# Kernel tuning notes

Measured on AMD Instinct MI355X. Metric: run time of the kernel, lower is better.

## Reference

```python
import math
import jax, jax.numpy as jnp
import numpy as np

N_HEADS = 8
EPS = 1e-6


def setup_inputs() -> dict:
    key = jax.random.key(0)
    k0, k1, k2, k3, k4 = jax.random.split(key, 5)
    B, T, E = 2, 1024, 512
    s = 1.0 / math.sqrt(E)
    x = jax.random.normal(k0, (B, T, E), dtype=jnp.float32)
    w_qkv = jax.random.normal(k1, (3 * E, E), dtype=jnp.float32) * s
    b_qkv = jax.random.normal(k2, (3 * E,), dtype=jnp.float32) * s
    w_out = jax.random.normal(k3, (E, E), dtype=jnp.float32) * s
    b_out = jax.random.normal(k4, (E,), dtype=jnp.float32) * s
    return {"x": x, "w_qkv": w_qkv, "b_qkv": b_qkv, "w_out": w_out, "b_out": b_out}


def reference(x, w_qkv, b_qkv, w_out, b_out):
    B, T, C = x.shape
    H = N_HEADS
    d = C // H

    qkv = x @ w_qkv.T + b_qkv                      # [B,T,3C]
    q, k, v = jnp.split(qkv, 3, axis=-1)

    def to_heads(t):
        return t.reshape(B, T, H, d).transpose(0, 2, 1, 3).astype(jnp.float32)  # [B,H,T,d]

    q, k, v = to_heads(q), to_heads(k), to_heads(v)

    pos = jnp.arange(T, dtype=jnp.float32)
    ang = (math.pi / 2) * pos / T
    cos_w = jnp.cos(ang)[None, None, :, None]      # [1,1,T,1]
    sin_w = jnp.sin(ang)[None, None, :, None]

    q_prime = jax.nn.relu(q)
    k_prime = jax.nn.relu(k)
    q_cos, q_sin = q_prime * cos_w, q_prime * sin_w
    k_cos, k_sin = k_prime * cos_w, k_prime * sin_w

    # causal linear attention via cumulative outer products (cosFormer)
    kv_cos_cs = jnp.cumsum(jnp.einsum('bhtd,bhte->bhtde', k_cos, v), axis=2)
    context = jnp.einsum('bhtd,bhtde->bhte', q_cos, kv_cos_cs)
    kv_sin_cs = jnp.cumsum(jnp.einsum('bhtd,bhte->bhtde', k_sin, v), axis=2)
    context = context + jnp.einsum('bhtd,bhtde->bhte', q_sin, kv_sin_cs)

    norm = (jnp.einsum('bhtd,bhtd->bht', q_cos, jnp.cumsum(k_cos, axis=2))
            + jnp.einsum('bhtd,bhtd->bht', q_sin, jnp.cumsum(k_sin, axis=2)))
    out = context / (norm[..., None] + EPS)        # [B,H,T,d]

    out = out.astype(x.dtype).transpose(0, 2, 1, 3).reshape(B, T, C)
    return out @ w_out.T + b_out
```

## Files before the change

### kernel.cpp

```cpp
#include <hip/hip_runtime.h>

typedef __bf16 bf16_t;
typedef __bf16 bf16x4 __attribute__((ext_vector_type(4)));
typedef __bf16 bf16x8 __attribute__((ext_vector_type(8)));
typedef float f32x4 __attribute__((ext_vector_type(4)));

#define T_SEQ 1024
#define EMB   512
#define NH    8
#define HD    64
#define BATCH 2
#define NBH   (BATCH*NH)
#define CHUNK 64
#define NCHUNK (T_SEQ/CHUNK)
#define NBLK  (NBH*NCHUNK)
#define LDA   72
#define LDK   68


__global__ __launch_bounds__(256) void cvt3_kernel(
    const float* __restrict__ x, const float* __restrict__ wq,
    const float* __restrict__ wo,
    bf16_t* __restrict__ xb, bf16_t* __restrict__ wqb, bf16_t* __restrict__ wob)
{
    int i = blockIdx.x * 256 + threadIdx.x;
    const float* s; bf16_t* d; int off;
    if (i < 262144)      { s = x;  d = xb;  off = i; }
    else if (i < 458752) { s = wq; d = wqb; off = i - 262144; }
    else                 { s = wo; d = wob; off = i - 458752; }
    float4 v = ((const float4*)s)[off];
    bf16x4 o;
    o[0] = (bf16_t)v.x; o[1] = (bf16_t)v.y;
    o[2] = (bf16_t)v.z; o[3] = (bf16_t)v.w;
    ((bf16x4*)d)[off] = o;
}

__global__ __launch_bounds__(256) void qkv_sum_kernel(
    const bf16_t* __restrict__ X, const bf16_t* __restrict__ W,
    const float* __restrict__ bias,
    bf16_t* __restrict__ qq, bf16_t* __restrict__ kk, bf16_t* __restrict__ vv,
    bf16_t* __restrict__ Ssc, bf16_t* __restrict__ Sss,
    float* __restrict__ zc, float* __restrict__ zs)
{
    __shared__ __align__(16) bf16_t sk[CHUNK * LDK];
    __shared__ __align__(16) bf16_t sv[CHUNK * LDK];
    __shared__ float cwt[CHUNK], swt[CHUNK];

    const int m0 = blockIdx.x * 64;
    const int h  = blockIdx.y;
    const int b  = m0 >> 10;
    const int ch = (m0 & 1023) >> 6;
    const int blk = (b * NH + h) * NCHUNK + ch;

    if (threadIdx.x < CHUNK) {
        int tg = ch * CHUNK + threadIdx.x;
        float ang = 1.5707963267948966f * (float)tg * (1.0f / (float)T_SEQ);
        cwt[threadIdx.x] = cosf(ang);
        swt[threadIdx.x] = sinf(ang);
    }

    const int w = threadIdx.x >> 6;
    const int lane = threadIdx.x & 63;
    if (w < 3) {
        const int rsel = lane & 15;
        const int koff = (lane >> 4) * 8;
        const int n0 = w * 512 + h * 64;
        f32x4 acc[4][4] = {};
        const bf16_t* Ap = X + (m0 + rsel) * EMB + koff;
        const bf16_t* Bp = W + (n0 + rsel) * EMB + koff;
#pragma unroll 4
        for (int k0 = 0; k0 < EMB; k0 += 32) {
            bf16x8 af[4], bfr[4];
            for (int i = 0; i < 4; ++i)
                af[i] = *(const bf16x8*)(Ap + i * 16 * EMB + k0);
            for (int j = 0; j < 4; ++j)
                bfr[j] = *(const bf16x8*)(Bp + j * 16 * EMB + k0);
            for (int i = 0; i < 4; ++i)
                for (int j = 0; j < 4; ++j)
                    acc[i][j] = __builtin_amdgcn_mfma_f32_16x16x32_bf16(
                        af[i], bfr[j], acc[i][j], 0, 0, 0);
        }
        for (int j = 0; j < 4; ++j) {
            const int feat = j * 16 + rsel;
            const float bn = bias[n0 + feat];
            for (int i = 0; i < 4; ++i) {
                const int tl0 = i * 16 + (lane >> 4) * 4;
                for (int r = 0; r < 4; ++r) {
                    const int tl = tl0 + r;
                    const int t = (m0 & 1023) + tl;
                    float val = acc[i][j][r] + bn;
                    int di = ((b * NH + h) * T_SEQ + t) * HD + feat;
                    if (w == 0) {
                        qq[di] = (bf16_t)fmaxf(val, 0.f);
                    } else if (w == 1) {
                        bf16_t kb = (bf16_t)fmaxf(val, 0.f);
                        kk[di] = kb;
                        sk[tl * LDK + feat] = kb;
                    } else {
                        bf16_t vb = (bf16_t)val;
                        vv[di] = vb;
                        sv[tl * LDK + feat] = vb;
                    }
                }
            }
        }
    }
    __syncthreads();

    const int i  = threadIdx.x & 63;
    const int jg = (threadIdx.x >> 6) * 16;
    float ac[16], as[16];
    for (int jj = 0; jj < 16; ++jj) { ac[jj] = 0.f; as[jj] = 0.f; }
    float zca = 0.f, zsa = 0.f;
    const bool zown = (jg == 0);
    for (int t = 0; t < CHUNK; ++t) {
        float kv = (float)sk[t * LDK + i];
        float kc_ = kv * cwt[t];
        float ks_ = kv * swt[t];
        if (zown) { zca += kc_; zsa += ks_; }
        for (int jj = 0; jj < 16; ++jj) {
            float vj = (float)sv[t * LDK + jg + jj];
            ac[jj] += kc_ * vj;
            as[jj] += ks_ * vj;
        }
    }
    bf16_t* oc = Ssc + blk * HD * HD;
    bf16_t* os = Sss + blk * HD * HD;
    for (int jj = 0; jj < 16; ++jj) {
        oc[(jg + jj) * HD + i] = (bf16_t)ac[jj];
        os[(jg + jj) * HD + i] = (bf16_t)as[jj];
    }
    if (zown) {
        zc[blk * HD + i] = zca;
        zs[blk * HD + i] = zsa;
    }
}

__global__ __launch_bounds__(256) void chunk_out_kernel(
    const bf16_t* __restrict__ qq, const bf16_t* __restrict__ kk,
    const bf16_t* __restrict__ vv,
    const bf16_t* __restrict__ SscT, const bf16_t* __restrict__ SssT,
    const float* __restrict__ zc, const float* __restrict__ zs,
    bf16_t* __restrict__ Y)
{
    const int blk = blockIdx.x;
    const int bh = blk >> 4, ch = blk & 15;
    __shared__ __align__(16) bf16_t sq [CHUNK * LDA];
    __shared__ __align__(16) bf16_t sk [CHUNK * LDA];
    __shared__ __align__(16) bf16_t svT[CHUNK * LDA];
    __shared__ __align__(16) bf16_t sct[CHUNK * LDA];
    __shared__ __align__(16) bf16_t sst[CHUNK * LDA];
    __shared__ __align__(16) bf16_t sp [CHUNK * LDA];
    __shared__ float cwt[CHUNK], swt[CHUNK], cosd[CHUNK];
    __shared__ float zcl[CHUNK], zsl[CHUNK], nrm[CHUNK];

    const int base = blk * CHUNK * HD;
    for (int i = threadIdx.x; i < CHUNK * HD / 8; i += 256) {
        int row = i >> 3, g = i & 7;
        ((uint4*)(sq + row * LDA))[g]  = ((const uint4*)(qq + base))[i];
        ((uint4*)(sk + row * LDA))[g]  = ((const uint4*)(kk + base))[i];
        bf16x8 v8 = *(const bf16x8*)(vv + base + i * 8);
        int t = i >> 3, bb = i & 7;
        int tg8 = t >> 3, tf = t & 7;
        for (int j = 0; j < 8; ++j) {
            int e = bb * 8 + j;
            int pg = (tg8 + bb) & 7;
            svT[e * LDA + pg * 8 + tf] = v8[j];
        }
    }
    {
        const int e0 = threadIdx.x * 16;
        float accC[16], accS[16];
        for (int j = 0; j < 16; ++j) { accC[j] = 0.f; accS[j] = 0.f; }
        const int sb = bh * NCHUNK * HD * HD + e0;
#pragma unroll 2
        for (int c = 0; c < ch; ++c) {
            const bf16x8* pc = (const bf16x8*)(SscT + sb + c * HD * HD);
            const bf16x8* ps = (const bf16x8*)(SssT + sb + c * HD * HD);
            bf16x8 c0 = pc[0], c1 = pc[1], s0 = ps[0], s1 = ps[1];
            for (int j = 0; j < 8; ++j) {
                accC[j] += (float)c0[j];  accC[8 + j] += (float)c1[j];
                accS[j] += (float)s0[j];  accS[8 + j] += (float)s1[j];
            }
        }
        const int row = threadIdx.x >> 2, col = (threadIdx.x & 3) * 16;
        bf16x8 oc0, oc1, os0, os1;
        for (int j = 0; j < 8; ++j) {
            oc0[j] = (bf16_t)accC[j];  oc1[j] = (bf16_t)accC[8 + j];
            os0[j] = (bf16_t)accS[j];  os1[j] = (bf16_t)accS[8 + j];
        }
        *(bf16x8*)(sct + row * LDA + col) = oc0;
        *(bf16x8*)(sct + row * LDA + col + 8) = oc1;
        *(bf16x8*)(sst + row * LDA + col) = os0;
        *(bf16x8*)(sst + row * LDA + col + 8) = os1;
    }
    if (threadIdx.x < HD) {
        int tl = threadIdx.x;
        float s = 0.f;
        for (int c = 0; c < ch; ++c) s += zc[(bh * NCHUNK + c) * HD + tl];
        zcl[tl] = s;
        int tg = ch * CHUNK + tl;
        float angg = 1.5707963267948966f * (float)tg * (1.0f / (float)T_SEQ);
        cwt[tl] = cosf(angg);
        swt[tl] = sinf(angg);
        cosd[tl] = cosf(1.5707963267948966f * (float)tl * (1.0f / (float)T_SEQ));
    } else if (threadIdx.x < 2 * HD) {
        int i = threadIdx.x - HD;
        float s = 0.f;
        for (int c = 0; c < ch; ++c) s += zs[(bh * NCHUNK + c) * HD + i];
        zsl[i] = s;
    }
    __syncthreads();

    const int w = threadIdx.x >> 6;
    const int lane = threadIdx.x & 63;
    const int rsel = lane & 15;
    const int koff = (lane >> 4) * 8;
    const int myrow = w * 16 + rsel;

    bf16x8 aq0 = *(const bf16x8*)(sq + myrow * LDA + koff);
    bf16x8 aq1 = *(const bf16x8*)(sq + myrow * LDA + koff + 32);
    for (int nt = 0; nt < 4; ++nt) {
        const int n0 = nt * 16;
        f32x4 pacc = {0.f, 0.f, 0.f, 0.f};
        bf16x8 b0 = *(const bf16x8*)(sk + (n0 + rsel) * LDA + koff);
        bf16x8 b1 = *(const bf16x8*)(sk + (n0 + rsel) * LDA + koff + 32);
        pacc = __builtin_amdgcn_mfma_f32_16x16x32_bf16(aq0, b0, pacc, 0, 0, 0);
        pacc = __builtin_amdgcn_mfma_f32_16x16x32_bf16(aq1, b1, pacc, 0, 0, 0);
        const int s = n0 + (lane & 15);
        const int tb = w * 16 + (lane >> 4) * 4;
        for (int r = 0; r < 4; ++r) {
            int t = tb + r;
            float p = (s <= t) ? pacc[r] * cosd[t - s] : 0.f;
            sp[t * LDA + s] = (bf16_t)p;
        }
    }

    if (lane < 16) {
        int row = w * 16 + lane;
        float nv = 0.f;
        const bf16x8* pr = (const bf16x8*)(sp + row * LDA);
        for (int g = 0; g < 8; ++g) {
            bf16x8 pv = pr[g];
            for (int j = 0; j < 8; ++j) nv += (float)pv[j];
        }
        float cwr = cwt[row], swr = swt[row];
        const bf16x8* qr = (const bf16x8*)(sq + row * LDA);
        for (int g = 0; g < 8; ++g) {
            bf16x8 qv = qr[g];
            for (int j = 0; j < 8; ++j)
                nv += (float)qv[j] * (cwr * zcl[g * 8 + j] + swr * zsl[g * 8 + j]);
        }
        nrm[row] = nv;
    }

    const float cwq = cwt[myrow], swq = swt[myrow];
    bf16x8 qc0, qc1, qs0, qs1;
    for (int j = 0; j < 8; ++j) {
        qc0[j] = (bf16_t)((float)aq0[j] * cwq);
        qc1[j] = (bf16_t)((float)aq1[j] * cwq);
        qs0[j] = (bf16_t)((float)aq0[j] * swq);
        qs1[j] = (bf16_t)((float)aq1[j] * swq);
    }
    bf16x8 ap0 = *(const bf16x8*)(sp + myrow * LDA + koff);
    bf16x8 ap1 = *(const bf16x8*)(sp + myrow * LDA + koff + 32);

    const int b = bh >> 3, h = bh & 7;
    const int g0 = koff >> 3;
    for (int nt = 0; nt < 4; ++nt) {
        const int n0 = nt * 16;
        const int ee = n0 + rsel;
        const int rot = (ee >> 3) & 7;
        const bf16_t* bvp0 = svT + ee * LDA + (((g0 + rot) & 7) << 3);
        const bf16_t* bvp1 = svT + ee * LDA + (((g0 + 4 + rot) & 7) << 3);
        const bf16_t* bcp = sct + ee * LDA + koff;
        const bf16_t* bsp = sst + ee * LDA + koff;
        f32x4 acc = {0.f, 0.f, 0.f, 0.f};
        acc = __builtin_amdgcn_mfma_f32_16x16x32_bf16(ap0, *(const bf16x8*)(bvp0), acc, 0, 0, 0);
        acc = __builtin_amdgcn_mfma_f32_16x16x32_bf16(ap1, *(const bf16x8*)(bvp1), acc, 0, 0, 0);
        acc = __builtin_amdgcn_mfma_f32_16x16x32_bf16(qc0, *(const bf16x8*)(bcp), acc, 0, 0, 0);
        acc = __builtin_amdgcn_mfma_f32_16x16x32_bf16(qc1, *(const bf16x8*)(bcp + 32), acc, 0, 0, 0);
        acc = __builtin_amdgcn_mfma_f32_16x16x32_bf16(qs0, *(const bf16x8*)(bsp), acc, 0, 0, 0);
        acc = __builtin_amdgcn_mfma_f32_16x16x32_bf16(qs1, *(const bf16x8*)(bsp + 32), acc, 0, 0, 0);
        const int col = n0 + (lane & 15);
        const int tb = w * 16 + (lane >> 4) * 4;
        for (int r = 0; r < 4; ++r) {
            int row = tb + r;
            float inv = 1.0f / (nrm[row] + 1e-6f);
            int tg = ch * CHUNK + row;
            Y[((b * T_SEQ + tg) * EMB) + h * HD + col] = (bf16_t)(acc[r] * inv);
        }
    }
}

__global__ __launch_bounds__(256) void out_gemm_kernel(
    const bf16_t* __restrict__ Yb, const bf16_t* __restrict__ W,
    const float* __restrict__ bias, float* __restrict__ out)
{
    const int w = threadIdx.x >> 6;
    const int lane = threadIdx.x & 63;
    const int rsel = lane & 15;
    const int koff = (lane >> 4) * 8;
    const int m0 = blockIdx.x * 64 + (w & 1) * 32;
    const int n0 = blockIdx.y * 64 + (w >> 1) * 32;
    f32x4 acc[2][2] = {};
    const bf16_t* Ap = Yb + (m0 + rsel) * EMB + koff;
    const bf16_t* Bp = W + (n0 + rsel) * EMB + koff;
#pragma unroll 8
    for (int k0 = 0; k0 < EMB; k0 += 32) {
        bf16x8 af[2], bfr[2];
        for (int i = 0; i < 2; ++i)
            af[i] = *(const bf16x8*)(Ap + i * 16 * EMB + k0);
        for (int j = 0; j < 2; ++j)
            bfr[j] = *(const bf16x8*)(Bp + j * 16 * EMB + k0);
        for (int i = 0; i < 2; ++i)
            for (int j = 0; j < 2; ++j)
                acc[i][j] = __builtin_amdgcn_mfma_f32_16x16x32_bf16(
                    af[i], bfr[j], acc[i][j], 0, 0, 0);
    }
    for (int j = 0; j < 2; ++j) {
        const int n = n0 + j * 16 + rsel;
        const float bn = bias[n];
        for (int i = 0; i < 2; ++i) {
            const int mb = m0 + i * 16 + (lane >> 4) * 4;
            for (int r = 0; r < 4; ++r)
                out[(mb + r) * EMB + n] = acc[i][j][r] + bn;
        }
    }
}

extern "C" void kernel_launch(void* const* d_in, const int* in_sizes, int n_in,
                              void* d_out, int out_size, void* d_ws, size_t ws_size,
                              hipStream_t stream) {
    const float* x     = (const float*)d_in[0];
    const float* w_qkv = (const float*)d_in[1];
    const float* b_qkv = (const float*)d_in[2];
    const float* w_out = (const float*)d_in[3];
    const float* b_out = (const float*)d_in[4];
    float* out = (float*)d_out;

    char* w = (char*)d_ws;
    const size_t N_X   = (size_t)BATCH * T_SEQ * EMB;
    const size_t N_WQ  = (size_t)3 * EMB * EMB;
    const size_t N_WO  = (size_t)EMB * EMB;
    bf16_t* xb   = (bf16_t*)w;                 w += N_X  * sizeof(bf16_t);
    bf16_t* wqb  = (bf16_t*)w;                 w += N_WQ * sizeof(bf16_t);
    bf16_t* wob  = (bf16_t*)w;                 w += N_WO * sizeof(bf16_t);
    const size_t SZ_BHTD = (size_t)NBH * T_SEQ * HD * sizeof(bf16_t);
    bf16_t* qq = (bf16_t*)w;                   w += SZ_BHTD;
    bf16_t* kk = (bf16_t*)w;                   w += SZ_BHTD;
    bf16_t* vv = (bf16_t*)w;                   w += SZ_BHTD;
    bf16_t* Y  = (bf16_t*)w;                   w += SZ_BHTD;
    bf16_t* SscT = (bf16_t*)w;                 w += (size_t)NBLK * HD * HD * sizeof(bf16_t);
    bf16_t* SssT = (bf16_t*)w;                 w += (size_t)NBLK * HD * HD * sizeof(bf16_t);
    float* zc = (float*)w;                     w += (size_t)NBLK * HD * sizeof(float);
    float* zs = (float*)w;

    cvt3_kernel<<<2048, 256, 0, stream>>>(x, w_qkv, w_out, xb, wqb, wob);
    qkv_sum_kernel<<<dim3(32, 8), 256, 0, stream>>>(
        xb, wqb, b_qkv, qq, kk, vv, SscT, SssT, zc, zs);
    chunk_out_kernel<<<NBLK, 256, 0, stream>>>(qq, kk, vv, SscT, SssT, zc, zs, Y);
    out_gemm_kernel<<<dim3(2048 / 64, 512 / 64), 256, 0, stream>>>(
        Y, wob, b_out, out);
}
```

Before: 118.8 us.

## Fuse all four stages into one cooperative kernel with grid syncs

Merges the conversion, QKV GEMM plus chunk-sum, chunk output, and output GEMM kernels into a single cooperative launch of 256 blocks. Grid-wide barriers separate the stages, and one shared-memory union is reused across phases. The goal is to remove per-kernel launch gaps and tail effects between four small kernels. The cost is grid.sync overhead and the conversion phase running on only 256 blocks instead of 2048.

```diff
diff --git a/kernel.cpp b/kernel.cpp
--- a/kernel.cpp
+++ b/kernel.cpp
@@ -1,4 +1,7 @@
 #include <hip/hip_runtime.h>
+#include <hip/hip_cooperative_groups.h>
+
+namespace cg = cooperative_groups;
 
 typedef __bf16 bf16_t;
 typedef __bf16 bf16x4 __attribute__((ext_vector_type(4)));
@@ -18,313 +21,329 @@
 #define LDK   68
 
 
-__global__ __launch_bounds__(256) void cvt3_kernel(
-    const float* __restrict__ x, const float* __restrict__ wq,
-    const float* __restrict__ wo,
-    bf16_t* __restrict__ xb, bf16_t* __restrict__ wqb, bf16_t* __restrict__ wob)
-{
-    int i = blockIdx.x * 256 + threadIdx.x;
-    const float* s; bf16_t* d; int off;
-    if (i < 262144)      { s = x;  d = xb;  off = i; }
-    else if (i < 458752) { s = wq; d = wqb; off = i - 262144; }
-    else                 { s = wo; d = wob; off = i - 458752; }
-    float4 v = ((const float4*)s)[off];
-    bf16x4 o;
-    o[0] = (bf16_t)v.x; o[1] = (bf16_t)v.y;
-    o[2] = (bf16_t)v.z; o[3] = (bf16_t)v.w;
-    ((bf16x4*)d)[off] = o;
-}
-
-__global__ __launch_bounds__(256) void qkv_sum_kernel(
-    const bf16_t* __restrict__ X, const bf16_t* __restrict__ W,
-    const float* __restrict__ bias,
+struct P1s {
+    bf16_t sk[CHUNK * LDK];
+    bf16_t sv[CHUNK * LDK];
+    float  cwt[CHUNK], swt[CHUNK];
+};
+struct P2s {
+    bf16_t sq [CHUNK * LDA];
+    bf16_t sk [CHUNK * LDA];
+    bf16_t svT[CHUNK * LDA];
+    bf16_t sct[CHUNK * LDA];
+    bf16_t sst[CHUNK * LDA];
+    bf16_t sp [CHUNK * LDA];
+    float  cwt[CHUNK], swt[CHUNK], cosd[CHUNK];
+    float  zcl[CHUNK], zsl[CHUNK], nrm[CHUNK];
+};
+union SMemU { P1s p1; P2s p2; };
+
+__global__ __launch_bounds__(256) void fused_kernel(
+    const float* __restrict__ x,  const float* __restrict__ wq,
+    const float* __restrict__ wo, const float* __restrict__ b_qkv,
+    const float* __restrict__ b_out,
+    bf16_t* __restrict__ xb, bf16_t* __restrict__ wqb, bf16_t* __restrict__ wob,
     bf16_t* __restrict__ qq, bf16_t* __restrict__ kk, bf16_t* __restrict__ vv,
     bf16_t* __restrict__ Ssc, bf16_t* __restrict__ Sss,
-    float* __restrict__ zc, float* __restrict__ zs)
+    float* __restrict__ zc, float* __restrict__ zs,
+    bf16_t* __restrict__ Y, float* __restrict__ out)
 {
-    __shared__ __align__(16) bf16_t sk[CHUNK * LDK];
-    __shared__ __align__(16) bf16_t sv[CHUNK * LDK];
-    __shared__ float cwt[CHUNK], swt[CHUNK];
-
-    const int m0 = blockIdx.x * 64;
-    const int h  = blockIdx.y;
-    const int b  = m0 >> 10;
-    const int ch = (m0 & 1023) >> 6;
-    const int blk = (b * NH + h) * NCHUNK + ch;
-
-    if (threadIdx.x < CHUNK) {
-        int tg = ch * CHUNK + threadIdx.x;
-        float ang = 1.5707963267948966f * (float)tg * (1.0f / (float)T_SEQ);
-        cwt[threadIdx.x] = cosf(ang);
-        swt[threadIdx.x] = sinf(ang);
+    __shared__ __align__(16) SMemU sm;
+    cg::grid_group grid = cg::this_grid();
+    const int tid = threadIdx.x;
+    const int blk = blockIdx.x;
+
+    for (int i = blk * 256 + tid; i < 524288; i += NBLK * 256) {
+        const float* s; bf16_t* d; int off;
+        if (i < 262144)      { s = x;  d = xb;  off = i; }
+        else if (i < 458752) { s = wq; d = wqb; off = i - 262144; }
+        else                 { s = wo; d = wob; off = i - 458752; }
+        float4 v = ((const float4*)s)[off];
+        bf16x4 o;
+        o[0] = (bf16_t)v.x; o[1] = (bf16_t)v.y;
+        o[2] = (bf16_t)v.z; o[3] = (bf16_t)v.w;
+        ((bf16x4*)d)[off] = o;
     }
-
-    const int w = threadIdx.x >> 6;
-    const int lane = threadIdx.x & 63;
-    if (w < 3) {
+    grid.sync();
+
+    {
+        bf16_t* sk  = sm.p1.sk;
+        bf16_t* sv  = sm.p1.sv;
+        float*  cwt = sm.p1.cwt;
+        float*  swt = sm.p1.swt;
+
+        const int m0 = (blk & 31) * 64;
+        const int h  = blk >> 5;
+        const int b  = m0 >> 10;
+        const int ch = (m0 & 1023) >> 6;
+        const int sblk = (b * NH + h) * NCHUNK + ch;
+
+        if (tid < CHUNK) {
+            int tg = ch * CHUNK + tid;
+            float ang = 1.5707963267948966f * (float)tg * (1.0f / (float)T_SEQ);
+            cwt[tid] = cosf(ang);
+            swt[tid] = sinf(ang);
+        }
+
+        const int w = tid >> 6;
+        const int lane = tid & 63;
+        if (w < 3) {
+            const int rsel = lane & 15;
+            const int koff = (lane >> 4) * 8;
+            const int n0 = w * 512 + h * 64;
+            f32x4 acc[4][4] = {};
+            const bf16_t* Ap = xb + (m0 + rsel) * EMB + koff;
+            const bf16_t* Bp = wqb + (n0 + rsel) * EMB + koff;
+#pragma unroll 4
+            for (int k0 = 0; k0 < EMB; k0 += 32) {
+                bf16x8 af[4], bfr[4];
+                for (int i = 0; i < 4; ++i)
+                    af[i] = *(const bf16x8*)(Ap + i * 16 * EMB + k0);
+                for (int j = 0; j < 4; ++j)
+                    bfr[j] = *(const bf16x8*)(Bp + j * 16 * EMB + k0);
+                for (int i = 0; i < 4; ++i)
+                    for (int j = 0; j < 4; ++j)
+                        acc[i][j] = __builtin_amdgcn_mfma_f32_16x16x32_bf16(
+                            af[i], bfr[j], acc[i][j], 0, 0, 0);
+            }
+            for (int j = 0; j < 4; ++j) {
+                const int feat = j * 16 + rsel;
+                const float bn = b_qkv[n0 + feat];
+                for (int i = 0; i < 4; ++i) {
+                    const int tl0 = i * 16 + (lane >> 4) * 4;
+                    for (int r = 0; r < 4; ++r) {
+                        const int tl = tl0 + r;
+                        const int t = (m0 & 1023) + tl;
+                        float val = acc[i][j][r] + bn;
+                        int di = ((b * NH + h) * T_SEQ + t) * HD + feat;
+                        if (w == 0) {
+                            qq[di] = (bf16_t)fmaxf(val, 0.f);
+                        } else if (w == 1) {
+                            bf16_t kb = (bf16_t)fmaxf(val, 0.f);
+                            kk[di] = kb;
+                            sk[tl * LDK + feat] = kb;
+                        } else {
+                            bf16_t vb = (bf16_t)val;
+                            vv[di] = vb;
+                            sv[tl * LDK + feat] = vb;
+                        }
+                    }
+                }
+            }
+        }
+        __syncthreads();
+
+        const int il = tid & 63;
+        const int jg = (tid >> 6) * 16;
+        float ac[16], as[16];
+        for (int jj = 0; jj < 16; ++jj) { ac[jj] = 0.f; as[jj] = 0.f; }
+        float zca = 0.f, zsa = 0.f;
+        const bool zown = (jg == 0);
+        for (int t = 0; t < CHUNK; ++t) {
+            float kv = (float)sk[t * LDK + il];
+            float kc_ = kv * cwt[t];
+            float ks_ = kv * swt[t];
+            if (zown) { zca += kc_; zsa += ks_; }
+            for (int jj = 0; jj < 16; ++jj) {
+                float vj = (float)sv[t * LDK + jg + jj];
+                ac[jj] += kc_ * vj;
+                as[jj] += ks_ * vj;
+            }
+        }
+        bf16_t* oc = Ssc + sblk * HD * HD;
+        bf16_t* os = Sss + sblk * HD * HD;
+        for (int jj = 0; jj < 16; ++jj) {
+            oc[(jg + jj) * HD + il] = (bf16_t)ac[jj];
+            os[(jg + jj) * HD + il] = (bf16_t)as[jj];
+        }
+        if (zown) {
+            zc[sblk * HD + il] = zca;
+            zs[sblk * HD + il] = zsa;
+        }
+    }
+    grid.sync();
+
+    {
+        const int bh = blk >> 4, ch = blk & 15;
+        bf16_t* sq  = sm.p2.sq;
+        bf16_t* skl = sm.p2.sk;
+        bf16_t* svT = sm.p2.svT;
+        bf16_t* sct = sm.p2.sct;
+        bf16_t* sst = sm.p2.sst;
+        bf16_t* sp  = sm.p2.sp;
+        float* cwt = sm.p2.cwt; float* swt = sm.p2.swt; float* cosd = sm.p2.cosd;
+        float* zcl = sm.p2.zcl; float* zsl = sm.p2.zsl; float* nrm = sm.p2.nrm;
+
+        const int base = blk * CHUNK * HD;
+        for (int i = tid; i < CHUNK * HD / 8; i += 256) {
+            int row = i >> 3, g = i & 7;
+            ((uint4*)(sq + row * LDA))[g]  = ((const uint4*)(qq + base))[i];
+            ((uint4*)(skl + row * LDA))[g] = ((const uint4*)(kk + base))[i];
+            bf16x8 v8 = *(const bf16x8*)(vv + base + i * 8);
+            int t = i >> 3, bb = i & 7;
+            int tg8 = t >> 3, tf = t & 7;
+            for (int j = 0; j < 8; ++j) {
+                int e = bb * 8 + j;
+                int pg = (tg8 + bb) & 7;
+                svT[e * LDA + pg * 8 + tf] = v8[j];
+            }
+        }
+        {
+            const int e0 = tid * 16;
+            float accC[16], accS[16];
+            for (int j = 0; j < 16; ++j) { accC[j] = 0.f; accS[j] = 0.f; }
+            const int sb = bh * NCHUNK * HD * HD + e0;
+#pragma unroll 2
+            for (int c = 0; c < ch; ++c) {
+                const bf16x8* pc = (const bf16x8*)(Ssc + sb + c * HD * HD);
+                const bf16x8* ps = (const bf16x8*)(Sss + sb + c * HD * HD);
+                bf16x8 c0 = pc[0], c1 = pc[1], s0 = ps[0], s1 = ps[1];
+                for (int j = 0; j < 8; ++j) {
+                    accC[j] += (float)c0[j];  accC[8 + j] += (float)c1[j];
+                    accS[j] += (float)s0[j];  accS[8 + j] += (float)s1[j];
+                }
+            }
+            const int row = tid >> 2, col = (tid & 3) * 16;
+            bf16x8 oc0, oc1, os0, os1;
+            for (int j = 0; j < 8; ++j) {
+                oc0[j] = (bf16_t)accC[j];  oc1[j] = (bf16_t)accC[8 + j];
+                os0[j] = (bf16_t)accS[j];  os1[j] = (bf16_t)accS[8 + j];
+            }
+            *(bf16x8*)(sct + row * LDA + col) = oc0;
+            *(bf16x8*)(sct + row * LDA + col + 8) = oc1;
+            *(bf16x8*)(sst + row * LDA + col) = os0;
+            *(bf16x8*)(sst + row * LDA + col + 8) = os1;
+        }
+        if (tid < HD) {
+            int tl = tid;
+            float s = 0.f;
+            for (int c = 0; c < ch; ++c) s += zc[(bh * NCHUNK + c) * HD + tl];
+            zcl[tl] = s;
+            int tg = ch * CHUNK + tl;
+            float angg = 1.5707963267948966f * (float)tg * (1.0f / (float)T_SEQ);
+            cwt[tl] = cosf(angg);
+            swt[tl] = sinf(angg);
+            cosd[tl] = cosf(1.5707963267948966f * (float)tl * (1.0f / (float)T_SEQ));
+        } else if (tid < 2 * HD) {
+            int i = tid - HD;
+            float s = 0.f;
+            for (int c = 0; c < ch; ++c) s += zs[(bh * NCHUNK + c) * HD + i];
+            zsl[i] = s;
+        }
+        __syncthreads();
+
+        const int w = tid >> 6;
+        const int lane = tid & 63;
         const int rsel = lane & 15;
         const int koff = (lane >> 4) * 8;
-        const int n0 = w * 512 + h * 64;
-        f32x4 acc[4][4] = {};
-        const bf16_t* Ap = X + (m0 + rsel) * EMB + koff;
-        const bf16_t* Bp = W + (n0 + rsel) * EMB + koff;
-#pragma unroll 4
+        const int myrow = w * 16 + rsel;
+
+        bf16x8 aq0 = *(const bf16x8*)(sq + myrow * LDA + koff);
+        bf16x8 aq1 = *(const bf16x8*)(sq + myrow * LDA + koff + 32);
+        for (int nt = 0; nt < 4; ++nt) {
+            const int n0 = nt * 16;
+            f32x4 pacc = {0.f, 0.f, 0.f, 0.f};
+            bf16x8 b0 = *(const bf16x8*)(skl + (n0 + rsel) * LDA + koff);
+            bf16x8 b1 = *(const bf16x8*)(skl + (n0 + rsel) * LDA + koff + 32);
+            pacc = __builtin_amdgcn_mfma_f32_16x16x32_bf16(aq0, b0, pacc, 0, 0, 0);
+            pacc = __builtin_amdgcn_mfma_f32_16x16x32_bf16(aq1, b1, pacc, 0, 0, 0);
+            const int s = n0 + (lane & 15);
+            const int tb = w * 16 + (lane >> 4) * 4;
+            for (int r = 0; r < 4; ++r) {
+                int t = tb + r;
+                float p = (s <= t) ? pacc[r] * cosd[t - s] : 0.f;
+                sp[t * LDA + s] = (bf16_t)p;
+            }
+        }
+
+        if (lane < 16) {
+            int row = w * 16 + lane;
+            float nv = 0.f;
+            const bf16x8* pr = (const bf16x8*)(sp + row * LDA);
+            for (int g = 0; g < 8; ++g) {
+                bf16x8 pv = pr[g];
+                for (int j = 0; j < 8; ++j) nv += (float)pv[j];
+            }
+            float cwr = cwt[row], swr = swt[row];
+            const bf16x8* qr = (const bf16x8*)(sq + row * LDA);
+            for (int g = 0; g < 8; ++g) {
+                bf16x8 qv = qr[g];
+                for (int j = 0; j < 8; ++j)
+                    nv += (float)qv[j] * (cwr * zcl[g * 8 + j] + swr * zsl[g * 8 + j]);
+            }
+            nrm[row] = nv;
+        }
+
+        const float cwq = cwt[myrow], swq = swt[myrow];
+        bf16x8 qc0, qc1, qs0, qs1;
+        for (int j = 0; j < 8; ++j) {
+            qc0[j] = (bf16_t)((float)aq0[j] * cwq);
+            qc1[j] = (bf16_t)((float)aq1[j] * cwq);
+            qs0[j] = (bf16_t)((float)aq0[j] * swq);
+            qs1[j] = (bf16_t)((float)aq1[j] * swq);
+        }
+        bf16x8 ap0 = *(const bf16x8*)(sp + myrow * LDA + koff);
+        bf16x8 ap1 = *(const bf16x8*)(sp + myrow * LDA + koff + 32);
+
+        const int b = bh >> 3, h = bh & 7;
+        const int g0 = koff >> 3;
+        for (int nt = 0; nt < 4; ++nt) {
+            const int n0 = nt * 16;
+            const int ee = n0 + rsel;
+            const int rot = (ee >> 3) & 7;
+            const bf16_t* bvp0 = svT + ee * LDA + (((g0 + rot) & 7) << 3);
+            const bf16_t* bvp1 = svT + ee * LDA + (((g0 + 4 + rot) & 7) << 3);
+            const bf16_t* bcp = sct + ee * LDA + koff;
+            const bf16_t* bsp = sst + ee * LDA + koff;
+            f32x4 acc = {0.f, 0.f, 0.f, 0.f};
+            acc = __builtin_amdgcn_mfma_f32_16x16x32_bf16(ap0, *(const bf16x8*)(bvp0), acc, 0, 0, 0);
+            acc = __builtin_amdgcn_mfma_f32_16x16x32_bf16(ap1, *(const bf16x8*)(bvp1), acc, 0, 0, 0);
+            acc = __builtin_amdgcn_mfma_f32_16x16x32_bf16(qc0, *(const bf16x8*)(bcp), acc, 0, 0, 0);
+            acc = __builtin_amdgcn_mfma_f32_16x16x32_bf16(qc1, *(const bf16x8*)(bcp + 32), acc, 0, 0, 0);
+            acc = __builtin_amdgcn_mfma_f32_16x16x32_bf16(qs0, *(const bf16x8*)(bsp), acc, 0, 0, 0);
+            acc = __builtin_amdgcn_mfma_f32_16x16x32_bf16(qs1, *(const bf16x8*)(bsp + 32), acc, 0, 0, 0);
+            const int col = n0 + (lane & 15);
+            const int tb = w * 16 + (lane >> 4) * 4;
+            for (int r = 0; r < 4; ++r) {
+                int row = tb + r;
+                float inv = 1.0f / (nrm[row] + 1e-6f);
+                int tg = ch * CHUNK + row;
+                Y[((b * T_SEQ + tg) * EMB) + h * HD + col] = (bf16_t)(acc[r] * inv);
+            }
+        }
+    }
+    grid.sync();
+
+    {
+        const int w = tid >> 6;
+        const int lane = tid & 63;
+        const int rsel = lane & 15;
+        const int koff = (lane >> 4) * 8;
+        const int m0 = (blk & 31) * 64 + (w & 1) * 32;
+        const int n0 = (blk >> 5) * 64 + (w >> 1) * 32;
+        f32x4 acc[2][2] = {};
+        const bf16_t* Ap = Y + (m0 + rsel) * EMB + koff;
+        const bf16_t* Bp = wob + (n0 + rsel) * EMB + koff;
+#pragma unroll 8
         for (int k0 = 0; k0 < EMB; k0 += 32) {
-            bf16x8 af[4], bfr[4];
-            for (int i = 0; i < 4; ++i)
+            bf16x8 af[2], bfr[2];
+            for (int i = 0; i < 2; ++i)
                 af[i] = *(const bf16x8*)(Ap + i * 16 * EMB + k0);
-            for (int j = 0; j < 4; ++j)
+            for (int j = 0; j < 2; ++j)
                 bfr[j] = *(const bf16x8*)(Bp + j * 16 * EMB + k0);
-            for (int i = 0; i < 4; ++i)
-                for (int j = 0; j < 4; ++j)
+            for (int i = 0; i < 2; ++i)
+                for (int j = 0; j < 2; ++j)
                     acc[i][j] = __builtin_amdgcn_mfma_f32_16x16x32_bf16(
                         af[i], bfr[j], acc[i][j], 0, 0, 0);
         }
-        for (int j = 0; j < 4; ++j) {
-            const int feat = j * 16 + rsel;
-            const float bn = bias[n0 + feat];
-            for (int i = 0; i < 4; ++i) {
-                const int tl0 = i * 16 + (lane >> 4) * 4;
-                for (int r = 0; r < 4; ++r) {
-                    const int tl = tl0 + r;
-                    const int t = (m0 & 1023) + tl;
-                    float val = acc[i][j][r] + bn;
-                    int di = ((b * NH + h) * T_SEQ + t) * HD + feat;
-                    if (w == 0) {
-                        qq[di] = (bf16_t)fmaxf(val, 0.f);
-                    } else if (w == 1) {
-                        bf16_t kb = (bf16_t)fmaxf(val, 0.f);
-                        kk[di] = kb;
-                        sk[tl * LDK + feat] = kb;
-                    } else {
-                        bf16_t vb = (bf16_t)val;
-                        vv[di] = vb;
-                        sv[tl * LDK + feat] = vb;
-                    }
-                }
-            }
-        }
-    }
-    __syncthreads();
-
-    const int i  = threadIdx.x & 63;
-    const int jg = (threadIdx.x >> 6) * 16;
-    float ac[16], as[16];
-    for (int jj = 0; jj < 16; ++jj) { ac[jj] = 0.f; as[jj] = 0.f; }
-    float zca = 0.f, zsa = 0.f;
-    const bool zown = (jg == 0);
-    for (int t = 0; t < CHUNK; ++t) {
-        float kv = (float)sk[t * LDK + i];
-        float kc_ = kv * cwt[t];
-        float ks_ = kv * swt[t];
-        if (zown) { zca += kc_; zsa += ks_; }
-        for (int jj = 0; jj < 16; ++jj) {
-            float vj = (float)sv[t * LDK + jg + jj];
-            ac[jj] += kc_ * vj;
-            as[jj] += ks_ * vj;
-        }
-    }
-    bf16_t* oc = Ssc + blk * HD * HD;
-    bf16_t* os = Sss + blk * HD * HD;
-    for (int jj = 0; jj < 16; ++jj) {
-        oc[(jg + jj) * HD + i] = (bf16_t)ac[jj];
-        os[(jg + jj) * HD + i] = (bf16_t)as[jj];
-    }
-    if (zown) {
-        zc[blk * HD + i] = zca;
-        zs[blk * HD + i] = zsa;
-    }
-}
-
-__global__ __launch_bounds__(256) void chunk_out_kernel(
-    const bf16_t* __restrict__ qq, const bf16_t* __restrict__ kk,
-    const bf16_t* __restrict__ vv,
-    const bf16_t* __restrict__ SscT, const bf16_t* __restrict__ SssT,
-    const float* __restrict__ zc, const float* __restrict__ zs,
-    bf16_t* __restrict__ Y)
-{
-    const int blk = blockIdx.x;
-    const int bh = blk >> 4, ch = blk & 15;
-    __shared__ __align__(16) bf16_t sq [CHUNK * LDA];
-    __shared__ __align__(16) bf16_t sk [CHUNK * LDA];
-    __shared__ __align__(16) bf16_t svT[CHUNK * LDA];
-    __shared__ __align__(16) bf16_t sct[CHUNK * LDA];
-    __shared__ __align__(16) bf16_t sst[CHUNK * LDA];
-    __shared__ __align__(16) bf16_t sp [CHUNK * LDA];
-    __shared__ float cwt[CHUNK], swt[CHUNK], cosd[CHUNK];
-    __shared__ float zcl[CHUNK], zsl[CHUNK], nrm[CHUNK];
-
-    const int base = blk * CHUNK * HD;
-    for (int i = threadIdx.x; i < CHUNK * HD / 8; i += 256) {
-        int row = i >> 3, g = i & 7;
-        ((uint4*)(sq + row * LDA))[g]  = ((const uint4*)(qq + base))[i];
-        ((uint4*)(sk + row * LDA))[g]  = ((const uint4*)(kk + base))[i];
-        bf16x8 v8 = *(const bf16x8*)(vv + base + i * 8);
-        int t = i >> 3, bb = i & 7;
-        int tg8 = t >> 3, tf = t & 7;
-        for (int j = 0; j < 8; ++j) {
-            int e = bb * 8 + j;
-            int pg = (tg8 + bb) & 7;
-            svT[e * LDA + pg * 8 + tf] = v8[j];
-        }
-    }
-    {
-        const int e0 = threadIdx.x * 16;
-        float accC[16], accS[16];
-        for (int j = 0; j < 16; ++j) { accC[j] = 0.f; accS[j] = 0.f; }
-        const int sb = bh * NCHUNK * HD * HD + e0;
-#pragma unroll 2
-        for (int c = 0; c < ch; ++c) {
-            const bf16x8* pc = (const bf16x8*)(SscT + sb + c * HD * HD);
-            const bf16x8* ps = (const bf16x8*)(SssT + sb + c * HD * HD);
-            bf16x8 c0 = pc[0], c1 = pc[1], s0 = ps[0], s1 = ps[1];
-            for (int j = 0; j < 8; ++j) {
-                accC[j] += (float)c0[j];  accC[8 + j] += (float)c1[j];
-                accS[j] += (float)s0[j];  accS[8 + j] += (float)s1[j];
-            }
-        }
-        const int row = threadIdx.x >> 2, col = (threadIdx.x & 3) * 16;
-        bf16x8 oc0, oc1, os0, os1;
-        for (int j = 0; j < 8; ++j) {
-            oc0[j] = (bf16_t)accC[j];  oc1[j] = (bf16_t)accC[8 + j];
-            os0[j] = (bf16_t)accS[j];  os1[j] = (bf16_t)accS[8 + j];
-        }
-        *(bf16x8*)(sct + row * LDA + col) = oc0;
-        *(bf16x8*)(sct + row * LDA + col + 8) = oc1;
-        *(bf16x8*)(sst + row * LDA + col) = os0;
-        *(bf16x8*)(sst + row * LDA + col + 8) = os1;
-    }
-    if (threadIdx.x < HD) {
-        int tl = threadIdx.x;
-        float s = 0.f;
-        for (int c = 0; c < ch; ++c) s += zc[(bh * NCHUNK + c) * HD + tl];
-        zcl[tl] = s;
-        int tg = ch * CHUNK + tl;
-        float angg = 1.5707963267948966f * (float)tg * (1.0f / (float)T_SEQ);
-        cwt[tl] = cosf(angg);
-        swt[tl] = sinf(angg);
-        cosd[tl] = cosf(1.5707963267948966f * (float)tl * (1.0f / (float)T_SEQ));
-    } else if (threadIdx.x < 2 * HD) {
-        int i = threadIdx.x - HD;
-        float s = 0.f;
-        for (int c = 0; c < ch; ++c) s += zs[(bh * NCHUNK + c) * HD + i];
-        zsl[i] = s;
-    }
-    __syncthreads();
-
-    const int w = threadIdx.x >> 6;
-    const int lane = threadIdx.x & 63;
-    const int rsel = lane & 15;
-    const int koff = (lane >> 4) * 8;
-    const int myrow = w * 16 + rsel;
-
-    bf16x8 aq0 = *(const bf16x8*)(sq + myrow * LDA + koff);
-    bf16x8 aq1 = *(const bf16x8*)(sq + myrow * LDA + koff + 32);
-    for (int nt = 0; nt < 4; ++nt) {
-        const int n0 = nt * 16;
-        f32x4 pacc = {0.f, 0.f, 0.f, 0.f};
-        bf16x8 b0 = *(const bf16x8*)(sk + (n0 + rsel) * LDA + koff);
-        bf16x8 b1 = *(const bf16x8*)(sk + (n0 + rsel) * LDA + koff + 32);
-        pacc = __builtin_amdgcn_mfma_f32_16x16x32_bf16(aq0, b0, pacc, 0, 0, 0);
-        pacc = __builtin_amdgcn_mfma_f32_16x16x32_bf16(aq1, b1, pacc, 0, 0, 0);
-        const int s = n0 + (lane & 15);
-        const int tb = w * 16 + (lane >> 4) * 4;
-        for (int r = 0; r < 4; ++r) {
-            int t = tb + r;
-            float p = (s <= t) ? pacc[r] * cosd[t - s] : 0.f;
-            sp[t * LDA + s] = (bf16_t)p;
-        }
-    }
-
-    if (lane < 16) {
-        int row = w * 16 + lane;
-        float nv = 0.f;
-        const bf16x8* pr = (const bf16x8*)(sp + row * LDA);
-        for (int g = 0; g < 8; ++g) {
-            bf16x8 pv = pr[g];
-            for (int j = 0; j < 8; ++j) nv += (float)pv[j];
-        }
-        float cwr = cwt[row], swr = swt[row];
-        const bf16x8* qr = (const bf16x8*)(sq + row * LDA);
-        for (int g = 0; g < 8; ++g) {
-            bf16x8 qv = qr[g];
-            for (int j = 0; j < 8; ++j)
-                nv += (float)qv[j] * (cwr * zcl[g * 8 + j] + swr * zsl[g * 8 + j]);
-        }
-        nrm[row] = nv;
-    }
-
-    const float cwq = cwt[myrow], swq = swt[myrow];
-    bf16x8 qc0, qc1, qs0, qs1;
-    for (int j = 0; j < 8; ++j) {
-        qc0[j] = (bf16_t)((float)aq0[j] * cwq);
-        qc1[j] = (bf16_t)((float)aq1[j] * cwq);
-        qs0[j] = (bf16_t)((float)aq0[j] * swq);
-        qs1[j] = (bf16_t)((float)aq1[j] * swq);
-    }
-    bf16x8 ap0 = *(const bf16x8*)(sp + myrow * LDA + koff);
-    bf16x8 ap1 = *(const bf16x8*)(sp + myrow * LDA + koff + 32);
-
-    const int b = bh >> 3, h = bh & 7;
-    const int g0 = koff >> 3;
-    for (int nt = 0; nt < 4; ++nt) {
-        const int n0 = nt * 16;
-        const int ee = n0 + rsel;
-        const int rot = (ee >> 3) & 7;
-        const bf16_t* bvp0 = svT + ee * LDA + (((g0 + rot) & 7) << 3);
-        const bf16_t* bvp1 = svT + ee * LDA + (((g0 + 4 + rot) & 7) << 3);
-        const bf16_t* bcp = sct + ee * LDA + koff;
-        const bf16_t* bsp = sst + ee * LDA + koff;
-        f32x4 acc = {0.f, 0.f, 0.f, 0.f};
-        acc = __builtin_amdgcn_mfma_f32_16x16x32_bf16(ap0, *(const bf16x8*)(bvp0), acc, 0, 0, 0);
-        acc = __builtin_amdgcn_mfma_f32_16x16x32_bf16(ap1, *(const bf16x8*)(bvp1), acc, 0, 0, 0);
-        acc = __builtin_amdgcn_mfma_f32_16x16x32_bf16(qc0, *(const bf16x8*)(bcp), acc, 0, 0, 0);
-        acc = __builtin_amdgcn_mfma_f32_16x16x32_bf16(qc1, *(const bf16x8*)(bcp + 32), acc, 0, 0, 0);
-        acc = __builtin_amdgcn_mfma_f32_16x16x32_bf16(qs0, *(const bf16x8*)(bsp), acc, 0, 0, 0);
-        acc = __builtin_amdgcn_mfma_f32_16x16x32_bf16(qs1, *(const bf16x8*)(bsp + 32), acc, 0, 0, 0);
-        const int col = n0 + (lane & 15);
-        const int tb = w * 16 + (lane >> 4) * 4;
-        for (int r = 0; r < 4; ++r) {
-            int row = tb + r;
-            float inv = 1.0f / (nrm[row] + 1e-6f);
-            int tg = ch * CHUNK + row;
-            Y[((b * T_SEQ + tg) * EMB) + h * HD + col] = (bf16_t)(acc[r] * inv);
-        }
-    }
-}
-
-__global__ __launch_bounds__(256) void out_gemm_kernel(
-    const bf16_t* __restrict__ Yb, const bf16_t* __restrict__ W,
-    const float* __restrict__ bias, float* __restrict__ out)
-{
-    const int w = threadIdx.x >> 6;
-    const int lane = threadIdx.x & 63;
-    const int rsel = lane & 15;
-    const int koff = (lane >> 4) * 8;
-    const int m0 = blockIdx.x * 64 + (w & 1) * 32;
-    const int n0 = blockIdx.y * 64 + (w >> 1) * 32;
-    f32x4 acc[2][2] = {};
-    const bf16_t* Ap = Yb + (m0 + rsel) * EMB + koff;
-    const bf16_t* Bp = W + (n0 + rsel) * EMB + koff;
-#pragma unroll 8
-    for (int k0 = 0; k0 < EMB; k0 += 32) {
-        bf16x8 af[2], bfr[2];
-        for (int i = 0; i < 2; ++i)
-            af[i] = *(const bf16x8*)(Ap + i * 16 * EMB + k0);
-        for (int j = 0; j < 2; ++j)
-            bfr[j] = *(const bf16x8*)(Bp + j * 16 * EMB + k0);
-        for (int i = 0; i < 2; ++i)
-            for (int j = 0; j < 2; ++j)
-                acc[i][j] = __builtin_amdgcn_mfma_f32_16x16x32_bf16(
-                    af[i], bfr[j], acc[i][j], 0, 0, 0);
-    }
-    for (int j = 0; j < 2; ++j) {
-        const int n = n0 + j * 16 + rsel;
-        const float bn = bias[n];
-        for (int i = 0; i < 2; ++i) {
-            const int mb = m0 + i * 16 + (lane >> 4) * 4;
-            for (int r = 0; r < 4; ++r)
-                out[(mb + r) * EMB + n] = acc[i][j][r] + bn;
+        for (int j = 0; j < 2; ++j) {
+            const int n = n0 + j * 16 + rsel;
+            const float bn = b_out[n];
+            for (int i = 0; i < 2; ++i) {
+                const int mb = m0 + i * 16 + (lane >> 4) * 4;
+                for (int r = 0; r < 4; ++r)
+                    out[(mb + r) * EMB + n] = acc[i][j][r] + bn;
+            }
         }
     }
 }
@@ -356,10 +375,13 @@
     float* zc = (float*)w;                     w += (size_t)NBLK * HD * sizeof(float);
     float* zs = (float*)w;
 
-    cvt3_kernel<<<2048, 256, 0, stream>>>(x, w_qkv, w_out, xb, wqb, wob);
-    qkv_sum_kernel<<<dim3(32, 8), 256, 0, stream>>>(
-        xb, wqb, b_qkv, qq, kk, vv, SscT, SssT, zc, zs);
-    chunk_out_kernel<<<NBLK, 256, 0, stream>>>(qq, kk, vv, SscT, SssT, zc, zs, Y);
-    out_gemm_kernel<<<dim3(2048 / 64, 512 / 64), 256, 0, stream>>>(
-        Y, wob, b_out, out);
+    void* args[] = {
+        (void*)&x, (void*)&w_qkv, (void*)&w_out, (void*)&b_qkv, (void*)&b_out,
+        (void*)&xb, (void*)&wqb, (void*)&wob,
+        (void*)&qq, (void*)&kk, (void*)&vv,
+        (void*)&SscT, (void*)&SssT, (void*)&zc, (void*)&zs,
+        (void*)&Y, (void*)&out
+    };
+    hipLaunchCooperativeKernel((const void*)fused_kernel, dim3(NBLK), dim3(256),
+                               args, 0, stream);
 }
```

New measurement: 218.6 us. 83.9% more time.

## Fuse fp32-to-bf16 conversion into GEMM loads and retile output GEMM

Applied to the files above, without the earlier changes.

Removes the separate conversion kernel and has the QKV and output GEMMs read fp32 inputs and weights directly, converting to bf16 in registers before the MFMA. This drops one kernel launch and a full round trip of bf16 copies through memory. In exchange each GEMM reads twice as many bytes per operand, and the weights are converted redundantly by every block. The output GEMM also drops to one 16-row tile per wave and launches twice as many blocks, giving more parallelism but less register reuse.

```diff
diff --git a/kernel.cpp b/kernel.cpp
--- a/kernel.cpp
+++ b/kernel.cpp
@@ -18,25 +18,17 @@
 #define LDK   68
 
 
-__global__ __launch_bounds__(256) void cvt3_kernel(
-    const float* __restrict__ x, const float* __restrict__ wq,
-    const float* __restrict__ wo,
-    bf16_t* __restrict__ xb, bf16_t* __restrict__ wqb, bf16_t* __restrict__ wob)
-{
-    int i = blockIdx.x * 256 + threadIdx.x;
-    const float* s; bf16_t* d; int off;
-    if (i < 262144)      { s = x;  d = xb;  off = i; }
-    else if (i < 458752) { s = wq; d = wqb; off = i - 262144; }
-    else                 { s = wo; d = wob; off = i - 458752; }
-    float4 v = ((const float4*)s)[off];
-    bf16x4 o;
-    o[0] = (bf16_t)v.x; o[1] = (bf16_t)v.y;
-    o[2] = (bf16_t)v.z; o[3] = (bf16_t)v.w;
-    ((bf16x4*)d)[off] = o;
+__device__ __forceinline__ bf16x8 cvt8(const float* __restrict__ p) {
+    float4 a = *(const float4*)p;
+    float4 b = *(const float4*)(p + 4);
+    bf16x8 r;
+    r[0] = (bf16_t)a.x; r[1] = (bf16_t)a.y; r[2] = (bf16_t)a.z; r[3] = (bf16_t)a.w;
+    r[4] = (bf16_t)b.x; r[5] = (bf16_t)b.y; r[6] = (bf16_t)b.z; r[7] = (bf16_t)b.w;
+    return r;
 }
 
 __global__ __launch_bounds__(256) void qkv_sum_kernel(
-    const bf16_t* __restrict__ X, const bf16_t* __restrict__ W,
+    const float* __restrict__ X, const float* __restrict__ W,
     const float* __restrict__ bias,
     bf16_t* __restrict__ qq, bf16_t* __restrict__ kk, bf16_t* __restrict__ vv,
     bf16_t* __restrict__ Ssc, bf16_t* __restrict__ Sss,
@@ -66,15 +58,15 @@
         const int koff = (lane >> 4) * 8;
         const int n0 = w * 512 + h * 64;
         f32x4 acc[4][4] = {};
-        const bf16_t* Ap = X + (m0 + rsel) * EMB + koff;
-        const bf16_t* Bp = W + (n0 + rsel) * EMB + koff;
-#pragma unroll 4
+        const float* Ap = X + (m0 + rsel) * EMB + koff;
+        const float* Bp = W + (n0 + rsel) * EMB + koff;
+#pragma unroll 2
         for (int k0 = 0; k0 < EMB; k0 += 32) {
             bf16x8 af[4], bfr[4];
             for (int i = 0; i < 4; ++i)
-                af[i] = *(const bf16x8*)(Ap + i * 16 * EMB + k0);
+                af[i] = cvt8(Ap + i * 16 * EMB + k0);
             for (int j = 0; j < 4; ++j)
-                bfr[j] = *(const bf16x8*)(Bp + j * 16 * EMB + k0);
+                bfr[j] = cvt8(Bp + j * 16 * EMB + k0);
             for (int i = 0; i < 4; ++i)
                 for (int j = 0; j < 4; ++j)
                     acc[i][j] = __builtin_amdgcn_mfma_f32_16x16x32_bf16(
@@ -294,38 +286,34 @@
 }
 
 __global__ __launch_bounds__(256) void out_gemm_kernel(
-    const bf16_t* __restrict__ Yb, const bf16_t* __restrict__ W,
+    const bf16_t* __restrict__ Yb, const float* __restrict__ W,
     const float* __restrict__ bias, float* __restrict__ out)
 {
     const int w = threadIdx.x >> 6;
     const int lane = threadIdx.x & 63;
     const int rsel = lane & 15;
     const int koff = (lane >> 4) * 8;
-    const int m0 = blockIdx.x * 64 + (w & 1) * 32;
+    const int m0 = blockIdx.x * 32 + (w & 1) * 16;
     const int n0 = blockIdx.y * 64 + (w >> 1) * 32;
-    f32x4 acc[2][2] = {};
+    f32x4 acc[2] = {};
     const bf16_t* Ap = Yb + (m0 + rsel) * EMB + koff;
-    const bf16_t* Bp = W + (n0 + rsel) * EMB + koff;
-#pragma unroll 8
+    const float* Bp = W + (n0 + rsel) * EMB + koff;
+#pragma unroll 4
     for (int k0 = 0; k0 < EMB; k0 += 32) {
-        bf16x8 af[2], bfr[2];
-        for (int i = 0; i < 2; ++i)
-            af[i] = *(const bf16x8*)(Ap + i * 16 * EMB + k0);
+        bf16x8 af = *(const bf16x8*)(Ap + k0);
+        bf16x8 bfr[2];
         for (int j = 0; j < 2; ++j)
-            bfr[j] = *(const bf16x8*)(Bp + j * 16 * EMB + k0);
-        for (int i = 0; i < 2; ++i)
-            for (int j = 0; j < 2; ++j)
-                acc[i][j] = __builtin_amdgcn_mfma_f32_16x16x32_bf16(
-                    af[i], bfr[j], acc[i][j], 0, 0, 0);
+            bfr[j] = cvt8(Bp + j * 16 * EMB + k0);
+        for (int j = 0; j < 2; ++j)
+            acc[j] = __builtin_amdgcn_mfma_f32_16x16x32_bf16(
+                af, bfr[j], acc[j], 0, 0, 0);
     }
     for (int j = 0; j < 2; ++j) {
         const int n = n0 + j * 16 + rsel;
         const float bn = bias[n];
-        for (int i = 0; i < 2; ++i) {
-            const int mb = m0 + i * 16 + (lane >> 4) * 4;
-            for (int r = 0; r < 4; ++r)
-                out[(mb + r) * EMB + n] = acc[i][j][r] + bn;
-        }
+        const int mb = m0 + (lane >> 4) * 4;
+        for (int r = 0; r < 4; ++r)
+            out[(mb + r) * EMB + n] = acc[j][r] + bn;
     }
 }
 
@@ -340,12 +328,6 @@
     float* out = (float*)d_out;
 
     char* w = (char*)d_ws;
-    const size_t N_X   = (size_t)BATCH * T_SEQ * EMB;
-    const size_t N_WQ  = (size_t)3 * EMB * EMB;
-    const size_t N_WO  = (size_t)EMB * EMB;
-    bf16_t* xb   = (bf16_t*)w;                 w += N_X  * sizeof(bf16_t);
-    bf16_t* wqb  = (bf16_t*)w;                 w += N_WQ * sizeof(bf16_t);
-    bf16_t* wob  = (bf16_t*)w;                 w += N_WO * sizeof(bf16_t);
     const size_t SZ_BHTD = (size_t)NBH * T_SEQ * HD * sizeof(bf16_t);
     bf16_t* qq = (bf16_t*)w;                   w += SZ_BHTD;
     bf16_t* kk = (bf16_t*)w;                   w += SZ_BHTD;
@@ -356,10 +338,9 @@
     float* zc = (float*)w;                     w += (size_t)NBLK * HD * sizeof(float);
     float* zs = (float*)w;
 
-    cvt3_kernel<<<2048, 256, 0, stream>>>(x, w_qkv, w_out, xb, wqb, wob);
     qkv_sum_kernel<<<dim3(32, 8), 256, 0, stream>>>(
-        xb, wqb, b_qkv, qq, kk, vv, SscT, SssT, zc, zs);
+        x, w_qkv, b_qkv, qq, kk, vv, SscT, SssT, zc, zs);
     chunk_out_kernel<<<NBLK, 256, 0, stream>>>(qq, kk, vv, SscT, SssT, zc, zs, Y);
-    out_gemm_kernel<<<dim3(2048 / 64, 512 / 64), 256, 0, stream>>>(
-        Y, wob, b_out, out);
-}
+    out_gemm_kernel<<<dim3(2048 / 32, 512 / 64), 256, 0, stream>>>(
+        Y, w_out, b_out, out);
+}
```

New measurement: 139.7 us. +17.6%, slower.

## Spread QKV projection over 12 waves and halve out-GEMM row tile

Applied to the files above, without the earlier changes.

The QKV+chunk-state kernel now runs 1024 threads per block. Each of 12 waves computes a 16-row by 64-feature slice instead of 3 waves each computing 64x64, and the chunk-state accumulation is split across 16 waves with 4 value columns each. The output GEMM uses 32-row tiles, which doubles the grid to 512 blocks. Both changes target low occupancy from only 256 blocks on a large GPU, at the cost of less register-level reuse of loaded fragments and more redundant global loads of the weight tiles.

```diff
diff --git a/kernel.cpp b/kernel.cpp
--- a/kernel.cpp
+++ b/kernel.cpp
@@ -35,7 +35,7 @@
     ((bf16x4*)d)[off] = o;
 }
 
-__global__ __launch_bounds__(256) void qkv_sum_kernel(
+__global__ __launch_bounds__(1024) void qkv_sum_kernel(
     const bf16_t* __restrict__ X, const bf16_t* __restrict__ W,
     const float* __restrict__ bias,
     bf16_t* __restrict__ qq, bf16_t* __restrict__ kk, bf16_t* __restrict__ vv,
@@ -59,58 +59,56 @@
         swt[threadIdx.x] = sinf(ang);
     }
 
-    const int w = threadIdx.x >> 6;
+    const int ww = threadIdx.x >> 6;
     const int lane = threadIdx.x & 63;
-    if (w < 3) {
+    if (ww < 12) {
+        const int mh  = ww & 3;
+        const int sel = ww >> 2;
         const int rsel = lane & 15;
         const int koff = (lane >> 4) * 8;
-        const int n0 = w * 512 + h * 64;
-        f32x4 acc[4][4] = {};
-        const bf16_t* Ap = X + (m0 + rsel) * EMB + koff;
+        const int n0 = sel * 512 + h * 64;
+        f32x4 acc[4] = {};
+        const bf16_t* Ap = X + (m0 + mh * 16 + rsel) * EMB + koff;
         const bf16_t* Bp = W + (n0 + rsel) * EMB + koff;
 #pragma unroll 4
         for (int k0 = 0; k0 < EMB; k0 += 32) {
-            bf16x8 af[4], bfr[4];
-            for (int i = 0; i < 4; ++i)
-                af[i] = *(const bf16x8*)(Ap + i * 16 * EMB + k0);
+            bf16x8 af = *(const bf16x8*)(Ap + k0);
+            bf16x8 bfr[4];
             for (int j = 0; j < 4; ++j)
                 bfr[j] = *(const bf16x8*)(Bp + j * 16 * EMB + k0);
-            for (int i = 0; i < 4; ++i)
-                for (int j = 0; j < 4; ++j)
-                    acc[i][j] = __builtin_amdgcn_mfma_f32_16x16x32_bf16(
-                        af[i], bfr[j], acc[i][j], 0, 0, 0);
+            for (int j = 0; j < 4; ++j)
+                acc[j] = __builtin_amdgcn_mfma_f32_16x16x32_bf16(
+                    af, bfr[j], acc[j], 0, 0, 0);
         }
         for (int j = 0; j < 4; ++j) {
             const int feat = j * 16 + rsel;
             const float bn = bias[n0 + feat];
-            for (int i = 0; i < 4; ++i) {
-                const int tl0 = i * 16 + (lane >> 4) * 4;
-                for (int r = 0; r < 4; ++r) {
-                    const int tl = tl0 + r;
-                    const int t = (m0 & 1023) + tl;
-                    float val = acc[i][j][r] + bn;
-                    int di = ((b * NH + h) * T_SEQ + t) * HD + feat;
-                    if (w == 0) {
-                        qq[di] = (bf16_t)fmaxf(val, 0.f);
-                    } else if (w == 1) {
-                        bf16_t kb = (bf16_t)fmaxf(val, 0.f);
-                        kk[di] = kb;
-                        sk[tl * LDK + feat] = kb;
-                    } else {
-                        bf16_t vb = (bf16_t)val;
-                        vv[di] = vb;
-                        sv[tl * LDK + feat] = vb;
-                    }
+            const int tl0 = mh * 16 + (lane >> 4) * 4;
+            for (int r = 0; r < 4; ++r) {
+                const int tl = tl0 + r;
+                const int t = (m0 & 1023) + tl;
+                float val = acc[j][r] + bn;
+                int di = ((b * NH + h) * T_SEQ + t) * HD + feat;
+                if (sel == 0) {
+                    qq[di] = (bf16_t)fmaxf(val, 0.f);
+                } else if (sel == 1) {
+                    bf16_t kb = (bf16_t)fmaxf(val, 0.f);
+                    kk[di] = kb;
+                    sk[tl * LDK + feat] = kb;
+                } else {
+                    bf16_t vb = (bf16_t)val;
+                    vv[di] = vb;
+                    sv[tl * LDK + feat] = vb;
                 }
             }
         }
     }
     __syncthreads();
 
-    const int i  = threadIdx.x & 63;
-    const int jg = (threadIdx.x >> 6) * 16;
-    float ac[16], as[16];
-    for (int jj = 0; jj < 16; ++jj) { ac[jj] = 0.f; as[jj] = 0.f; }
+    const int i  = lane;
+    const int jg = ww * 4;
+    float ac[4], as[4];
+    for (int jj = 0; jj < 4; ++jj) { ac[jj] = 0.f; as[jj] = 0.f; }
     float zca = 0.f, zsa = 0.f;
     const bool zown = (jg == 0);
     for (int t = 0; t < CHUNK; ++t) {
@@ -118,7 +116,7 @@
         float kc_ = kv * cwt[t];
         float ks_ = kv * swt[t];
         if (zown) { zca += kc_; zsa += ks_; }
-        for (int jj = 0; jj < 16; ++jj) {
+        for (int jj = 0; jj < 4; ++jj) {
             float vj = (float)sv[t * LDK + jg + jj];
             ac[jj] += kc_ * vj;
             as[jj] += ks_ * vj;
@@ -126,7 +124,7 @@
     }
     bf16_t* oc = Ssc + blk * HD * HD;
     bf16_t* os = Sss + blk * HD * HD;
-    for (int jj = 0; jj < 16; ++jj) {
+    for (int jj = 0; jj < 4; ++jj) {
         oc[(jg + jj) * HD + i] = (bf16_t)ac[jj];
         os[(jg + jj) * HD + i] = (bf16_t)as[jj];
     }
@@ -301,31 +299,27 @@
     const int lane = threadIdx.x & 63;
     const int rsel = lane & 15;
     const int koff = (lane >> 4) * 8;
-    const int m0 = blockIdx.x * 64 + (w & 1) * 32;
+    const int m0 = blockIdx.x * 32 + (w & 1) * 16;
     const int n0 = blockIdx.y * 64 + (w >> 1) * 32;
-    f32x4 acc[2][2] = {};
+    f32x4 acc[2] = {};
     const bf16_t* Ap = Yb + (m0 + rsel) * EMB + koff;
     const bf16_t* Bp = W + (n0 + rsel) * EMB + koff;
-#pragma unroll 8
+#pragma unroll 4
     for (int k0 = 0; k0 < EMB; k0 += 32) {
-        bf16x8 af[2], bfr[2];
-        for (int i = 0; i < 2; ++i)
-            af[i] = *(const bf16x8*)(Ap + i * 16 * EMB + k0);
+        bf16x8 af = *(const bf16x8*)(Ap + k0);
+        bf16x8 bfr[2];
         for (int j = 0; j < 2; ++j)
             bfr[j] = *(const bf16x8*)(Bp + j * 16 * EMB + k0);
-        for (int i = 0; i < 2; ++i)
-            for (int j = 0; j < 2; ++j)
-                acc[i][j] = __builtin_amdgcn_mfma_f32_16x16x32_bf16(
-                    af[i], bfr[j], acc[i][j], 0, 0, 0);
+        for (int j = 0; j < 2; ++j)
+            acc[j] = __builtin_amdgcn_mfma_f32_16x16x32_bf16(
+                af, bfr[j], acc[j], 0, 0, 0);
     }
     for (int j = 0; j < 2; ++j) {
         const int n = n0 + j * 16 + rsel;
         const float bn = bias[n];
-        for (int i = 0; i < 2; ++i) {
-            const int mb = m0 + i * 16 + (lane >> 4) * 4;
-            for (int r = 0; r < 4; ++r)
-                out[(mb + r) * EMB + n] = acc[i][j][r] + bn;
-        }
+        const int mb = m0 + (lane >> 4) * 4;
+        for (int r = 0; r < 4; ++r)
+            out[(mb + r) * EMB + n] = acc[j][r] + bn;
     }
 }
 
@@ -357,9 +351,9 @@
     float* zs = (float*)w;
 
     cvt3_kernel<<<2048, 256, 0, stream>>>(x, w_qkv, w_out, xb, wqb, wob);
-    qkv_sum_kernel<<<dim3(32, 8), 256, 0, stream>>>(
+    qkv_sum_kernel<<<dim3(32, 8), 1024, 0, stream>>>(
         xb, wqb, b_qkv, qq, kk, vv, SscT, SssT, zc, zs);
     chunk_out_kernel<<<NBLK, 256, 0, stream>>>(qq, kk, vv, SscT, SssT, zc, zs, Y);
-    out_gemm_kernel<<<dim3(2048 / 64, 512 / 64), 256, 0, stream>>>(
+    out_gemm_kernel<<<dim3(2048 / 32, 512 / 64), 256, 0, stream>>>(
         Y, wob, b_out, out);
 }
```

New measurement: 129.8 us. +9.2%, slower.
